# Kernel optimization log

Hardware: AMD Instinct MI355X
Metric: run time of the kernel (lower is better)

The kernel has to match this reference:

```python
import jax, jax.numpy as jnp
import numpy as np

B, DZ, DS, DH = 8192, 1024, 64, 4096

def setup_inputs() -> dict:
    key = jax.random.key(0)
    ks = jax.random.split(key, 8)
    r1 = 1.0 / np.sqrt(DZ)   # W1 init range (last dim dz)
    r2 = 1.0 / np.sqrt(DH)   # W2 init range (last dim dim_hidden)
    rc = 1.0 / np.sqrt(DS)   # C init range
    return {
        "z": jax.random.normal(ks[0], (B, DZ), jnp.float32),
        "s": jax.random.normal(ks[1], (B, DS), jnp.float32),
        "A": jnp.full((DZ,), 0.95, jnp.float32),
        "W1": jax.random.uniform(ks[2], (DH, DZ), jnp.float32, -r1, r1),
        "W2": jax.random.uniform(ks[3], (DZ, DH), jnp.float32, -r2, r2),
        "h1": jax.random.normal(ks[4], (DH,), jnp.float32),
        "h2": jax.random.normal(ks[5], (DZ,), jnp.float32),
        "C": jax.random.uniform(ks[6], (DZ, DS), jnp.float32, -rc, rc),
    }

def reference(z, s, A, W1, W2, h1, h2, C):
    # PLRNN step, W_trial=False, mean_center=False, noise=0:
    # z' = A*z + relu(z @ W1.T + h1) @ W2.T + h2 + s @ C.T
    z_activated = jax.nn.relu(z @ W1.T + h1)          # [B, DH]
    return A * z + z_activated @ W2.T + h2 + s @ C.T  # [B, DZ]
```

## Files before the change

kernel.cpp:

```cpp
#include <hip/hip_runtime.h>

#define BB 8192
#define DZ 1024
#define DS 64
#define DH 4096
#define KEXT (DH + DS)

typedef float floatx4 __attribute__((ext_vector_type(4)));
typedef __bf16 bf16x8 __attribute__((ext_vector_type(8)));
typedef __bf16 bf16x4 __attribute__((ext_vector_type(4)));
typedef __attribute__((address_space(1))) void* as1_void_ptr;
typedef __attribute__((address_space(3))) void* as3_void_ptr;

#define WAIT_VM0   3952
#define WAIT_VM6   3958
#define WAIT_LGKM0 49279

__device__ __forceinline__ void async_copy16(const void* g, void* l) {
    __builtin_amdgcn_global_load_lds((as1_void_ptr)g, (as3_void_ptr)l, 16, 0, 0);
}

__device__ __forceinline__ bf16x8 cvt8(float4 a, float4 b) {
    bf16x8 o = { (__bf16)a.x, (__bf16)a.y, (__bf16)a.z, (__bf16)a.w,
                 (__bf16)b.x, (__bf16)b.y, (__bf16)b.z, (__bf16)b.w };
    return o;
}


__global__ __launch_bounds__(256) void prep_all(
    const float* __restrict__ z, const float* __restrict__ W1,
    const float* __restrict__ W2, const float* __restrict__ C,
    const float* __restrict__ s,
    __bf16* __restrict__ zb, __bf16* __restrict__ W1b,
    __bf16* __restrict__ B2b, __bf16* __restrict__ Hb)
{
    constexpr int NC_Z  = (BB * DZ) / 8;
    constexpr int NC_W1 = (DH * DZ) / 8;
    constexpr int NC_B2 = (DZ * KEXT) / 8;
    constexpr int NC_S  = (BB * DS) / 8;
    constexpr int NC_TOT = NC_Z + NC_W1 + NC_B2 + NC_S;
    const int stride = gridDim.x * blockDim.x;
    for (int c = blockIdx.x * blockDim.x + threadIdx.x; c < NC_TOT; c += stride) {
        const float4* src;
        __bf16* dst;
        if (c < NC_Z) {
            src = (const float4*)z + (size_t)c * 2;
            dst = zb + (size_t)c * 8;
        } else if (c < NC_Z + NC_W1) {
            int i = c - NC_Z;
            src = (const float4*)W1 + (size_t)i * 2;
            dst = W1b + (size_t)i * 8;
        } else if (c < NC_Z + NC_W1 + NC_B2) {
            int i = c - (NC_Z + NC_W1);
            int j = i / 520, p = i - j * 520;
            int h = p * 8;
            const float* sp = (h < DH) ? (W2 + (size_t)j * DH + h)
                                       : (C  + (size_t)j * DS + (h - DH));
            src = (const float4*)sp;
            dst = B2b + (size_t)j * KEXT + h;
        } else {
            int i = c - (NC_Z + NC_W1 + NC_B2);
            int r = i >> 3, k = (i & 7) * 8;
            src = (const float4*)(s + (size_t)r * DS + k);
            dst = Hb + (size_t)r * KEXT + DH + k;
        }
        float4 a = src[0], b = src[1];
        *(bf16x8*)dst = cvt8(a, b);
    }
}

__global__ __launch_bounds__(512, 4) void gemm1_relu(
    const __bf16* __restrict__ Ag, const __bf16* __restrict__ Bg,
    const float* __restrict__ h1, __bf16* __restrict__ Hb)
{
    constexpr int ldA = DZ, ldB = DZ, KITER = DZ / 64;
    __shared__ __align__(16) __bf16 As[256 * 64];
    __shared__ __align__(16) __bf16 Bs[128 * 64];

    const int tid = threadIdx.x;
    const int wave = tid >> 6, lane = tid & 63;
    const int wm = wave >> 1, wn = wave & 1;
    const int row0 = blockIdx.x * 256;
    const int col0 = blockIdx.y * 128;

    const int csrc = ((tid & 3) ^ ((tid >> 3) & 3)) * 8;
    const __bf16* pA = Ag + (size_t)(row0 + (tid >> 2)) * ldA + csrc;
    const __bf16* pB = Bg + (size_t)(col0 + ((tid >> 2) & 127)) * ldB + csrc;
    __bf16* lA = As + wave * 512;
    __bf16* lB = Bs + wave * 512;

    const int cswz = ((lane >> 4) ^ ((lane >> 1) & 3)) * 8;
    const __bf16* Afrag = As + (wm * 64 + (lane & 15)) * 32 + cswz;
    const __bf16* Bfrag = Bs + (wn * 64 + (lane & 15)) * 32 + cswz;

    floatx4 acc[4][4];
#pragma unroll
    for (int i = 0; i < 4; ++i)
#pragma unroll
        for (int j = 0; j < 4; ++j) acc[i][j] = (floatx4)0.0f;

    for (int kt = 0; kt < KITER; ++kt) {
        const __bf16* ak = pA + kt * 64;
        const __bf16* bk = pB + kt * 64;
        async_copy16(ak,                           lA);
        async_copy16(ak + (size_t)128 * ldA,       lA + 4096);
        async_copy16(ak + 32,                      lA + 8192);
        async_copy16(ak + (size_t)128 * ldA + 32,  lA + 8192 + 4096);
        async_copy16(bk,                           lB);
        async_copy16(bk + 32,                      lB + 4096);
        __builtin_amdgcn_s_waitcnt(0);
        __syncthreads();

#pragma unroll
        for (int ks = 0; ks < 2; ++ks) {
            bf16x8 af[4], bfr[4];
#pragma unroll
            for (int i = 0; i < 4; ++i) af[i] = *(const bf16x8*)(Afrag + ks * 8192 + i * 16 * 32);
#pragma unroll
            for (int j = 0; j < 4; ++j) bfr[j] = *(const bf16x8*)(Bfrag + ks * 4096 + j * 16 * 32);
#pragma unroll
            for (int i = 0; i < 4; ++i)
#pragma unroll
                for (int j = 0; j < 4; ++j)
                    acc[i][j] = __builtin_amdgcn_mfma_f32_16x16x32_bf16(af[i], bfr[j], acc[i][j], 0, 0, 0);
        }
        __syncthreads();
    }

    const int r0 = row0 + wm * 64 + (lane >> 4) * 4;
    const int c0 = col0 + wn * 64 + (lane & 15);
#pragma unroll
    for (int i = 0; i < 4; ++i) {
#pragma unroll
        for (int j = 0; j < 4; ++j) {
            int c = c0 + j * 16;
            float bias = h1[c];
#pragma unroll
            for (int rg = 0; rg < 4; ++rg) {
                int r = r0 + i * 16 + rg;
                float v = acc[i][j][rg] + bias;
                v = v > 0.0f ? v : 0.0f;
                Hb[(size_t)r * KEXT + c] = (__bf16)v;
            }
        }
    }
}

__global__ __launch_bounds__(512, 2) void gemm2_out(
    const __bf16* __restrict__ Ag, const __bf16* __restrict__ Bg,
    const float* __restrict__ Adiag, const float* __restrict__ h2,
    const __bf16* __restrict__ zb, float* __restrict__ out)
{
    constexpr int ldA = KEXT, ldB = KEXT, KITER = KEXT / 64;
    __shared__ __align__(16) __bf16 As[2 * 256 * 64];
    __shared__ __align__(16) __bf16 Bs[2 * 128 * 64];

    const int tid = threadIdx.x;
    const int wave = tid >> 6, lane = tid & 63;
    const int wm = wave >> 1, wn = wave & 1;
    const int row0 = blockIdx.x * 256;
    const int col0 = blockIdx.y * 128;

    const int csrc = ((tid & 3) ^ ((tid >> 3) & 3)) * 8;
    const __bf16* pA = Ag + (size_t)(row0 + (tid >> 2)) * ldA + csrc;
    const __bf16* pB = Bg + (size_t)(col0 + ((tid >> 2) & 127)) * ldB + csrc;

    const int cswz = ((lane >> 4) ^ ((lane >> 1) & 3)) * 8;
    const __bf16* Afrag = As + (wm * 64 + (lane & 15)) * 32 + cswz;
    const __bf16* Bfrag = Bs + (wn * 64 + (lane & 15)) * 32 + cswz;

    floatx4 acc[4][4];
#pragma unroll
    for (int i = 0; i < 4; ++i)
#pragma unroll
        for (int j = 0; j < 4; ++j) acc[i][j] = (floatx4)0.0f;

    auto issue = [&](int kt, int q) {
        const __bf16* ak = pA + kt * 64;
        const __bf16* bk = pB + kt * 64;
        __bf16* lA = As + q * 16384 + wave * 512;
        __bf16* lB = Bs + q * 8192  + wave * 512;
        async_copy16(ak,                           lA);
        async_copy16(ak + (size_t)128 * ldA,       lA + 4096);
        async_copy16(ak + 32,                      lA + 8192);
        async_copy16(ak + (size_t)128 * ldA + 32,  lA + 8192 + 4096);
        async_copy16(bk,                           lB);
        async_copy16(bk + 32,                      lB + 4096);
    };

    issue(0, 0);

    for (int kt = 0; kt < KITER; ++kt) {
        const int p = kt & 1;
        if (kt + 1 < KITER) {
            issue(kt + 1, p ^ 1);
            __builtin_amdgcn_s_waitcnt(WAIT_VM6);
        } else {
            __builtin_amdgcn_s_waitcnt(WAIT_VM0);
        }
        __builtin_amdgcn_s_barrier();

#pragma unroll
        for (int ks = 0; ks < 2; ++ks) {
            const __bf16* Ab = Afrag + p * 16384 + ks * 8192;
            const __bf16* Bb = Bfrag + p * 8192  + ks * 4096;
            bf16x8 af[4], bfr[4];
#pragma unroll
            for (int i = 0; i < 4; ++i) af[i] = *(const bf16x8*)(Ab + i * 16 * 32);
#pragma unroll
            for (int j = 0; j < 4; ++j) bfr[j] = *(const bf16x8*)(Bb + j * 16 * 32);
#pragma unroll
            for (int i = 0; i < 4; ++i)
#pragma unroll
                for (int j = 0; j < 4; ++j)
                    acc[i][j] = __builtin_amdgcn_mfma_f32_16x16x32_bf16(af[i], bfr[j], acc[i][j], 0, 0, 0);
        }

        __builtin_amdgcn_s_waitcnt(WAIT_LGKM0);
        __builtin_amdgcn_s_barrier();
    }

    const int r0 = row0 + wm * 64 + (lane >> 4) * 4;
    const int c0 = col0 + wn * 64 + (lane & 15);
#pragma unroll
    for (int i = 0; i < 4; ++i) {
#pragma unroll
        for (int j = 0; j < 4; ++j) {
            const int c = c0 + j * 16;
            const float aj = Adiag[c];
            const float hj = h2[c];
#pragma unroll
            for (int rg = 0; rg < 4; ++rg) {
                const int r = r0 + i * 16 + rg;
                out[(size_t)r * DZ + c] =
                    acc[i][j][rg] + aj * (float)zb[(size_t)r * DZ + c] + hj;
            }
        }
    }
}


extern "C" void kernel_launch(void* const* d_in, const int* in_sizes, int n_in,
                              void* d_out, int out_size, void* d_ws, size_t ws_size,
                              hipStream_t stream) {
    const float* z  = (const float*)d_in[0];
    const float* s  = (const float*)d_in[1];
    const float* A  = (const float*)d_in[2];
    const float* W1 = (const float*)d_in[3];
    const float* W2 = (const float*)d_in[4];
    const float* h1 = (const float*)d_in[5];
    const float* h2 = (const float*)d_in[6];
    const float* C  = (const float*)d_in[7];
    float* out = (float*)d_out;

    char* ws = (char*)d_ws;
    size_t offHb  = 0;
    size_t offZb  = offHb  + (size_t)BB * KEXT * 2;
    size_t offW1b = offZb  + (size_t)BB * DZ * 2;
    size_t offB2b = offW1b + (size_t)DH * DZ * 2;
    __bf16* Hb  = (__bf16*)(ws + offHb);
    __bf16* zb  = (__bf16*)(ws + offZb);
    __bf16* W1b = (__bf16*)(ws + offW1b);
    __bf16* B2b = (__bf16*)(ws + offB2b);

    prep_all<<<2048, 256, 0, stream>>>(z, W1, W2, C, s, zb, W1b, B2b, Hb);
    gemm1_relu<<<dim3(BB / 256, DH / 128), 512, 0, stream>>>(zb, W1b, h1, Hb);
    gemm2_out<<<dim3(BB / 256, DZ / 128), 512, 0, stream>>>(Hb, B2b, A, h2, zb, out);
}
```

Measured before the change: 253.8 us.

## Fuse z fp32-to-bf16 conversion into GEMM1 A-tile load; read fp32 z in epilogue

The separate pass that converts z to bf16 is removed. GEMM1 now loads fp32 z straight from global memory through registers, converts it, and writes swizzled bf16 into LDS in place of the async global-to-LDS copy. The GEMM2 epilogue reads the original fp32 z, which also makes the A*z term more accurate. The cost is that GEMM1 rereads z in fp32 (twice the bytes) for each of its 32 column blocks and loses the async copy path, so the A-load latency is no longer hidden the same way.

```diff
diff --git a/kernel.cpp b/kernel.cpp
--- a/kernel.cpp
+++ b/kernel.cpp
@@ -28,30 +28,24 @@
 
 
 __global__ __launch_bounds__(256) void prep_all(
-    const float* __restrict__ z, const float* __restrict__ W1,
-    const float* __restrict__ W2, const float* __restrict__ C,
-    const float* __restrict__ s,
-    __bf16* __restrict__ zb, __bf16* __restrict__ W1b,
-    __bf16* __restrict__ B2b, __bf16* __restrict__ Hb)
+    const float* __restrict__ W1, const float* __restrict__ W2,
+    const float* __restrict__ C, const float* __restrict__ s,
+    __bf16* __restrict__ W1b, __bf16* __restrict__ B2b,
+    __bf16* __restrict__ Hb)
 {
-    constexpr int NC_Z  = (BB * DZ) / 8;
     constexpr int NC_W1 = (DH * DZ) / 8;
     constexpr int NC_B2 = (DZ * KEXT) / 8;
     constexpr int NC_S  = (BB * DS) / 8;
-    constexpr int NC_TOT = NC_Z + NC_W1 + NC_B2 + NC_S;
+    constexpr int NC_TOT = NC_W1 + NC_B2 + NC_S;
     const int stride = gridDim.x * blockDim.x;
     for (int c = blockIdx.x * blockDim.x + threadIdx.x; c < NC_TOT; c += stride) {
         const float4* src;
         __bf16* dst;
-        if (c < NC_Z) {
-            src = (const float4*)z + (size_t)c * 2;
-            dst = zb + (size_t)c * 8;
-        } else if (c < NC_Z + NC_W1) {
-            int i = c - NC_Z;
-            src = (const float4*)W1 + (size_t)i * 2;
-            dst = W1b + (size_t)i * 8;
-        } else if (c < NC_Z + NC_W1 + NC_B2) {
-            int i = c - (NC_Z + NC_W1);
+        if (c < NC_W1) {
+            src = (const float4*)W1 + (size_t)c * 2;
+            dst = W1b + (size_t)c * 8;
+        } else if (c < NC_W1 + NC_B2) {
+            int i = c - NC_W1;
             int j = i / 520, p = i - j * 520;
             int h = p * 8;
             const float* sp = (h < DH) ? (W2 + (size_t)j * DH + h)
@@ -59,7 +53,7 @@
             src = (const float4*)sp;
             dst = B2b + (size_t)j * KEXT + h;
         } else {
-            int i = c - (NC_Z + NC_W1 + NC_B2);
+            int i = c - (NC_W1 + NC_B2);
             int r = i >> 3, k = (i & 7) * 8;
             src = (const float4*)(s + (size_t)r * DS + k);
             dst = Hb + (size_t)r * KEXT + DH + k;
@@ -70,10 +64,10 @@
 }
 
 __global__ __launch_bounds__(512, 4) void gemm1_relu(
-    const __bf16* __restrict__ Ag, const __bf16* __restrict__ Bg,
+    const float* __restrict__ Az, const __bf16* __restrict__ Bg,
     const float* __restrict__ h1, __bf16* __restrict__ Hb)
 {
-    constexpr int ldA = DZ, ldB = DZ, KITER = DZ / 64;
+    constexpr int ldB = DZ, KITER = DZ / 64;
     __shared__ __align__(16) __bf16 As[256 * 64];
     __shared__ __align__(16) __bf16 Bs[128 * 64];
 
@@ -83,10 +77,12 @@
     const int row0 = blockIdx.x * 256;
     const int col0 = blockIdx.y * 128;
 
+    const float* az = Az + (size_t)(row0 + (tid >> 1)) * DZ + (tid & 1) * 32;
+    __bf16* aw = As + (tid & 1) * 8192 + (tid >> 1) * 32;
+    const int rsw = (tid >> 2) & 3;
+
     const int csrc = ((tid & 3) ^ ((tid >> 3) & 3)) * 8;
-    const __bf16* pA = Ag + (size_t)(row0 + (tid >> 2)) * ldA + csrc;
-    const __bf16* pB = Bg + (size_t)(col0 + ((tid >> 2) & 127)) * ldB + csrc;
-    __bf16* lA = As + wave * 512;
+    const __bf16* pB = Bg + (size_t)(col0 + (tid >> 2)) * ldB + csrc;
     __bf16* lB = Bs + wave * 512;
 
     const int cswz = ((lane >> 4) ^ ((lane >> 1) & 3)) * 8;
@@ -100,14 +96,16 @@
         for (int j = 0; j < 4; ++j) acc[i][j] = (floatx4)0.0f;
 
     for (int kt = 0; kt < KITER; ++kt) {
-        const __bf16* ak = pA + kt * 64;
         const __bf16* bk = pB + kt * 64;
-        async_copy16(ak,                           lA);
-        async_copy16(ak + (size_t)128 * ldA,       lA + 4096);
-        async_copy16(ak + 32,                      lA + 8192);
-        async_copy16(ak + (size_t)128 * ldA + 32,  lA + 8192 + 4096);
-        async_copy16(bk,                           lB);
-        async_copy16(bk + 32,                      lB + 4096);
+        async_copy16(bk,      lB);
+        async_copy16(bk + 32, lB + 4096);
+        const float* zk = az + kt * 64;
+#pragma unroll
+        for (int c = 0; c < 4; ++c) {
+            float4 a = *(const float4*)(zk + c * 8);
+            float4 b = *(const float4*)(zk + c * 8 + 4);
+            *(bf16x8*)(aw + ((c ^ rsw) << 3)) = cvt8(a, b);
+        }
         __builtin_amdgcn_s_waitcnt(0);
         __syncthreads();
 
@@ -149,7 +147,7 @@
 __global__ __launch_bounds__(512, 2) void gemm2_out(
     const __bf16* __restrict__ Ag, const __bf16* __restrict__ Bg,
     const float* __restrict__ Adiag, const float* __restrict__ h2,
-    const __bf16* __restrict__ zb, float* __restrict__ out)
+    const float* __restrict__ z, float* __restrict__ out)
 {
     constexpr int ldA = KEXT, ldB = KEXT, KITER = KEXT / 64;
     __shared__ __align__(16) __bf16 As[2 * 256 * 64];
@@ -233,7 +231,7 @@
             for (int rg = 0; rg < 4; ++rg) {
                 const int r = r0 + i * 16 + rg;
                 out[(size_t)r * DZ + c] =
-                    acc[i][j][rg] + aj * (float)zb[(size_t)r * DZ + c] + hj;
+                    acc[i][j][rg] + aj * z[(size_t)r * DZ + c] + hj;
             }
         }
     }
@@ -255,15 +253,13 @@
 
     char* ws = (char*)d_ws;
     size_t offHb  = 0;
-    size_t offZb  = offHb  + (size_t)BB * KEXT * 2;
-    size_t offW1b = offZb  + (size_t)BB * DZ * 2;
+    size_t offW1b = offHb  + (size_t)BB * KEXT * 2;
     size_t offB2b = offW1b + (size_t)DH * DZ * 2;
     __bf16* Hb  = (__bf16*)(ws + offHb);
-    __bf16* zb  = (__bf16*)(ws + offZb);
     __bf16* W1b = (__bf16*)(ws + offW1b);
     __bf16* B2b = (__bf16*)(ws + offB2b);
 
-    prep_all<<<2048, 256, 0, stream>>>(z, W1, W2, C, s, zb, W1b, B2b, Hb);
-    gemm1_relu<<<dim3(BB / 256, DH / 128), 512, 0, stream>>>(zb, W1b, h1, Hb);
-    gemm2_out<<<dim3(BB / 256, DZ / 128), 512, 0, stream>>>(Hb, B2b, A, h2, zb, out);
-}
+    prep_all<<<2048, 256, 0, stream>>>(W1, W2, C, s, W1b, B2b, Hb);
+    gemm1_relu<<<dim3(BB / 256, DH / 128), 512, 0, stream>>>(z, W1b, h1, Hb);
+    gemm2_out<<<dim3(BB / 256, DZ / 128), 512, 0, stream>>>(Hb, B2b, A, h2, z, out);
+}
```

Measured after the change: 355.6 us. +40.1%, slower.

## Software-pipeline gemm2 with half-tile staged async loads and MFMA priority

Applied to the files above, without the earlier changes.

Restructures the second GEMM's main loop into phases over half-K sub-tiles. Each phase issues the next chunk of global-to-LDS copies while MFMAs run, under s_setprio boosts and finer-grained waitcnt and barriers. The aim is better overlap of memory loads with matrix compute than the previous coarse double buffer. The epilogue now reads the fp32 z directly instead of the bf16 copy, which improves accuracy but adds epilogue read bandwidth. More barriers per iteration and a complex hand-unrolled tail add sync overhead and correctness risk.

```diff
diff --git a/kernel.cpp b/kernel.cpp
--- a/kernel.cpp
+++ b/kernel.cpp
@@ -8,11 +8,11 @@
 
 typedef float floatx4 __attribute__((ext_vector_type(4)));
 typedef __bf16 bf16x8 __attribute__((ext_vector_type(8)));
-typedef __bf16 bf16x4 __attribute__((ext_vector_type(4)));
 typedef __attribute__((address_space(1))) void* as1_void_ptr;
 typedef __attribute__((address_space(3))) void* as3_void_ptr;
 
 #define WAIT_VM0   3952
+#define WAIT_VM3   3955
 #define WAIT_VM6   3958
 #define WAIT_LGKM0 49279
 
@@ -146,14 +146,39 @@
     }
 }
 
+#define G2_PH(Q, KS, IH, STAGE_STMT, WVM) do {                                 \
+    const __bf16* Ab_ = Afrag + (Q)*16384 + (KS)*8192 + (IH)*1024;             \
+    bf16x8 af_[2];                                                             \
+    _Pragma("unroll")                                                          \
+    for (int i_ = 0; i_ < 2; ++i_) af_[i_] = *(const bf16x8*)(Ab_ + i_*512);   \
+    if ((IH) == 0) {                                                           \
+        const __bf16* Bb_ = Bfrag + (Q)*8192 + (KS)*4096;                      \
+        _Pragma("unroll")                                                      \
+        for (int j_ = 0; j_ < 4; ++j_) bfr[j_] = *(const bf16x8*)(Bb_ + j_*512);\
+    }                                                                          \
+    STAGE_STMT;                                                                \
+    __builtin_amdgcn_s_barrier();                                              \
+    __builtin_amdgcn_s_waitcnt(WAIT_LGKM0);                                    \
+    __builtin_amdgcn_s_setprio(1);                                             \
+    _Pragma("unroll")                                                          \
+    for (int i_ = 0; i_ < 2; ++i_)                                             \
+        _Pragma("unroll")                                                      \
+        for (int j_ = 0; j_ < 4; ++j_)                                         \
+            acc[(IH)*2+i_][j_] = __builtin_amdgcn_mfma_f32_16x16x32_bf16(      \
+                af_[i_], bfr[j_], acc[(IH)*2+i_][j_], 0, 0, 0);                \
+    __builtin_amdgcn_s_setprio(0);                                             \
+    if ((WVM) >= 0) __builtin_amdgcn_s_waitcnt(WVM);                           \
+    __builtin_amdgcn_s_barrier();                                              \
+} while (0)
+
 __global__ __launch_bounds__(512, 2) void gemm2_out(
     const __bf16* __restrict__ Ag, const __bf16* __restrict__ Bg,
     const float* __restrict__ Adiag, const float* __restrict__ h2,
-    const __bf16* __restrict__ zb, float* __restrict__ out)
+    const float* __restrict__ z, float* __restrict__ out)
 {
-    constexpr int ldA = KEXT, ldB = KEXT, KITER = KEXT / 64;
-    __shared__ __align__(16) __bf16 As[2 * 256 * 64];
-    __shared__ __align__(16) __bf16 Bs[2 * 128 * 64];
+    constexpr int ldA = KEXT, ldB = KEXT;
+    __shared__ __align__(16) __bf16 As[2 * 2 * 256 * 32];
+    __shared__ __align__(16) __bf16 Bs[2 * 2 * 128 * 32];
 
     const int tid = threadIdx.x;
     const int wave = tid >> 6, lane = tid & 63;
@@ -163,61 +188,61 @@
 
     const int csrc = ((tid & 3) ^ ((tid >> 3) & 3)) * 8;
     const __bf16* pA = Ag + (size_t)(row0 + (tid >> 2)) * ldA + csrc;
-    const __bf16* pB = Bg + (size_t)(col0 + ((tid >> 2) & 127)) * ldB + csrc;
+    const __bf16* pB = Bg + (size_t)(col0 + (tid >> 2)) * ldB + csrc;
 
     const int cswz = ((lane >> 4) ^ ((lane >> 1) & 3)) * 8;
     const __bf16* Afrag = As + (wm * 64 + (lane & 15)) * 32 + cswz;
     const __bf16* Bfrag = Bs + (wn * 64 + (lane & 15)) * 32 + cswz;
 
+    auto sA0 = [&](int t, int q) { const __bf16* a = pA + t * 64;
+        __bf16* d = As + q * 16384 + wave * 512;
+        async_copy16(a, d); async_copy16(a + (size_t)128 * ldA, d + 4096); };
+    auto sA1 = [&](int t, int q) { const __bf16* a = pA + t * 64 + 32;
+        __bf16* d = As + q * 16384 + 8192 + wave * 512;
+        async_copy16(a, d); async_copy16(a + (size_t)128 * ldA, d + 4096); };
+    auto sB0 = [&](int t, int q) { const __bf16* b = pB + t * 64;
+        __bf16* d = Bs + q * 8192 + wave * 512;
+        async_copy16(b, d); };
+    auto sB1 = [&](int t, int q) { const __bf16* b = pB + t * 64 + 32;
+        __bf16* d = Bs + q * 8192 + 4096 + wave * 512;
+        async_copy16(b, d); };
+
     floatx4 acc[4][4];
 #pragma unroll
     for (int i = 0; i < 4; ++i)
 #pragma unroll
         for (int j = 0; j < 4; ++j) acc[i][j] = (floatx4)0.0f;
-
-    auto issue = [&](int kt, int q) {
-        const __bf16* ak = pA + kt * 64;
-        const __bf16* bk = pB + kt * 64;
-        __bf16* lA = As + q * 16384 + wave * 512;
-        __bf16* lB = Bs + q * 8192  + wave * 512;
-        async_copy16(ak,                           lA);
-        async_copy16(ak + (size_t)128 * ldA,       lA + 4096);
-        async_copy16(ak + 32,                      lA + 8192);
-        async_copy16(ak + (size_t)128 * ldA + 32,  lA + 8192 + 4096);
-        async_copy16(bk,                           lB);
-        async_copy16(bk + 32,                      lB + 4096);
-    };
-
-    issue(0, 0);
-
-    for (int kt = 0; kt < KITER; ++kt) {
-        const int p = kt & 1;
-        if (kt + 1 < KITER) {
-            issue(kt + 1, p ^ 1);
-            __builtin_amdgcn_s_waitcnt(WAIT_VM6);
-        } else {
-            __builtin_amdgcn_s_waitcnt(WAIT_VM0);
-        }
-        __builtin_amdgcn_s_barrier();
-
-#pragma unroll
-        for (int ks = 0; ks < 2; ++ks) {
-            const __bf16* Ab = Afrag + p * 16384 + ks * 8192;
-            const __bf16* Bb = Bfrag + p * 8192  + ks * 4096;
-            bf16x8 af[4], bfr[4];
-#pragma unroll
-            for (int i = 0; i < 4; ++i) af[i] = *(const bf16x8*)(Ab + i * 16 * 32);
-#pragma unroll
-            for (int j = 0; j < 4; ++j) bfr[j] = *(const bf16x8*)(Bb + j * 16 * 32);
-#pragma unroll
-            for (int i = 0; i < 4; ++i)
-#pragma unroll
-                for (int j = 0; j < 4; ++j)
-                    acc[i][j] = __builtin_amdgcn_mfma_f32_16x16x32_bf16(af[i], bfr[j], acc[i][j], 0, 0, 0);
-        }
-
-        __builtin_amdgcn_s_waitcnt(WAIT_LGKM0);
-        __builtin_amdgcn_s_barrier();
+    bf16x8 bfr[4];
+
+    sA0(0, 0); sB0(0, 0); sA1(0, 0); sB1(0, 0);
+    sA0(1, 1); sB0(1, 1);
+    __builtin_amdgcn_s_waitcnt(WAIT_VM6);
+    __builtin_amdgcn_s_barrier();
+
+    for (int r = 0; r < 31; ++r) {
+        const int t1 = 2 * r + 1, t2 = 2 * r + 2, t3 = 2 * r + 3;
+        G2_PH(0, 0, 0, sA1(t1, 1), -1);
+        G2_PH(0, 0, 1, sB1(t1, 1), WAIT_VM6);
+        G2_PH(0, 1, 0, sA0(t2, 0), -1);
+        G2_PH(0, 1, 1, sB0(t2, 0), WAIT_VM6);
+        G2_PH(1, 0, 0, sA1(t2, 0), -1);
+        G2_PH(1, 0, 1, sB1(t2, 0), WAIT_VM6);
+        G2_PH(1, 1, 0, sA0(t3, 1), -1);
+        G2_PH(1, 1, 1, sB0(t3, 1), WAIT_VM6);
+    }
+    {
+        G2_PH(0, 0, 0, sA1(63, 1), -1);
+        G2_PH(0, 0, 1, sB1(63, 1), WAIT_VM6);
+        G2_PH(0, 1, 0, sA0(64, 0), -1);
+        G2_PH(0, 1, 1, sB0(64, 0), WAIT_VM6);
+        G2_PH(1, 0, 0, sA1(64, 0), -1);
+        G2_PH(1, 0, 1, sB1(64, 0), WAIT_VM6);
+        G2_PH(1, 1, 0, (void)0,    -1);
+        G2_PH(1, 1, 1, (void)0,    WAIT_VM3);
+        G2_PH(0, 0, 0, (void)0,    -1);
+        G2_PH(0, 0, 1, (void)0,    WAIT_VM0);
+        G2_PH(0, 1, 0, (void)0,    -1);
+        G2_PH(0, 1, 1, (void)0,    -1);
     }
 
     const int r0 = row0 + wm * 64 + (lane >> 4) * 4;
@@ -233,7 +258,7 @@
             for (int rg = 0; rg < 4; ++rg) {
                 const int r = r0 + i * 16 + rg;
                 out[(size_t)r * DZ + c] =
-                    acc[i][j][rg] + aj * (float)zb[(size_t)r * DZ + c] + hj;
+                    acc[i][j][rg] + aj * z[(size_t)r * DZ + c] + hj;
             }
         }
     }
@@ -265,5 +290,5 @@
 
     prep_all<<<2048, 256, 0, stream>>>(z, W1, W2, C, s, zb, W1b, B2b, Hb);
     gemm1_relu<<<dim3(BB / 256, DH / 128), 512, 0, stream>>>(zb, W1b, h1, Hb);
-    gemm2_out<<<dim3(BB / 256, DZ / 128), 512, 0, stream>>>(Hb, B2b, A, h2, zb, out);
-}
+    gemm2_out<<<dim3(BB / 256, DZ / 128), 512, 0, stream>>>(Hb, B2b, A, h2, z, out);
+}
```

Result: slower. 281.4 us (+10.9%).
